# Kernel optimization log

Measured on AMD Instinct MI355X. Metric: run time of the kernel, lower is better.

Reference implementation:

```python
import jax, jax.numpy as jnp
import numpy as np

NUM_ITER = 3  # routing iterations (canonical CapsNet)
EPS = 1e-12


def _conv(x, w, stride):
    return jax.lax.conv_general_dilated(
        x, w, (stride, stride), 'VALID',
        dimension_numbers=('NCHW', 'OIHW', 'NCHW'))


def _squash(t, axis=-1):
    sn = (t * t).sum(axis=axis, keepdims=True)
    return sn / (1.0 + sn) * t / jnp.sqrt(sn + EPS)


def _batchnorm(x, eps=1e-5):
    # fresh BatchNorm2d in training mode: batch stats, weight=1, bias=0, biased var
    m = x.mean((0, 2, 3), keepdims=True)
    v = ((x - m) ** 2).mean((0, 2, 3), keepdims=True)
    return (x - m) * jax.lax.rsqrt(v + eps)


def _branch(x, cw, cb, pw, pb, rw):
    # x: [B,1,H,W]; cw: [128,1,k,k]; pw: [8,32,128,k,k]; rw: [10,R,8,16]
    y = jax.nn.relu(_conv(x, cw, 1) + cb[None, :, None, None])
    y = _batchnorm(y)
    nc, oc = pw.shape[0], pw.shape[1]  # 8 capsules, 32 channels each
    p = _conv(y, pw.reshape(nc * oc, pw.shape[2], pw.shape[3], pw.shape[4]), 2)
    p = p + pb.reshape(-1)[None, :, None, None]          # [B,256,h,w]
    B = p.shape[0]
    u = jnp.transpose(p.reshape(B, nc, -1), (0, 2, 1))   # [B,R,8], R=32*h*w
    u = _squash(u, axis=-1)
    priors = jnp.einsum('bri,nrio->nbro', u, rw)         # [10,B,R,16]
    b = jnp.zeros(priors.shape[:3] + (1,), priors.dtype)  # [10,B,R,1]
    for i in range(NUM_ITER):
        c = jax.nn.softmax(b, axis=2)                    # over route nodes
        v = _squash((c * priors).sum(axis=2, keepdims=True))  # [10,B,1,16]
        if i < NUM_ITER - 1:
            b = b + (priors * v).sum(axis=-1, keepdims=True)
    v = jnp.transpose(v[:, :, 0, :], (1, 0, 2))          # [B,10,16]
    return jnp.sqrt((v * v).sum(-1) + EPS)               # [B,10] capsule lengths


def setup_inputs() -> dict:
    key = jax.random.key(0)
    ks = jax.random.split(key, 16)
    s = 0.05
    return {
        'x': jax.random.normal(ks[0], (256, 1, 28, 28), jnp.float32),
        'conv1_w': jax.random.normal(ks[1], (128, 1, 3, 3), jnp.float32) * s,
        'conv1_b': jnp.zeros((128,), jnp.float32),
        'prim1_w': jax.random.normal(ks[2], (8, 32, 128, 3, 3), jnp.float32) * s,
        'prim1_b': jnp.zeros((8, 32), jnp.float32),
        'digit1_w': jax.random.normal(ks[3], (10, 128, 8, 16), jnp.float32),
        'conv2_w': jax.random.normal(ks[4], (128, 1, 5, 5), jnp.float32) * s,
        'conv2_b': jnp.zeros((128,), jnp.float32),
        'prim2_w': jax.random.normal(ks[5], (8, 32, 128, 5, 5), jnp.float32) * s,
        'prim2_b': jnp.zeros((8, 32), jnp.float32),
        'digit2_w': jax.random.normal(ks[6], (10, 288, 8, 16), jnp.float32),
        'conv3_w': jax.random.normal(ks[7], (128, 1, 9, 9), jnp.float32) * s,
        'conv3_b': jnp.zeros((128,), jnp.float32),
        'prim3_w': jax.random.normal(ks[8], (8, 32, 128, 9, 9), jnp.float32) * s,
        'prim3_b': jnp.zeros((8, 32), jnp.float32),
        'digit3_w': jax.random.normal(ks[9], (10, 1152, 8, 16), jnp.float32),
    }


def reference(x, conv1_w, conv1_b, prim1_w, prim1_b, digit1_w,
              conv2_w, conv2_b, prim2_w, prim2_b, digit2_w,
              conv3_w, conv3_b, prim3_w, prim3_b, digit3_w):
    img = x[:, 0]                                   # [B,28,28]
    B = img.shape[0]
    x3 = img                                        # 28x28
    x2 = img.reshape(B, 14, 2, 14, 2).mean((2, 4))  # 14x14 pyramid level
    x1 = x2.reshape(B, 7, 2, 7, 2).mean((2, 4))     # 7x7 pyramid level
    l1 = _branch(x1[:, None], conv1_w, conv1_b, prim1_w, prim1_b, digit1_w)
    l2 = _branch(x2[:, None], conv2_w, conv2_b, prim2_w, prim2_b, digit2_w)
    l3 = _branch(x3[:, None], conv3_w, conv3_b, prim3_w, prim3_b, digit3_w)
    return jax.nn.softmax(l1 + l2 + l3, axis=-1)    # [B,10]
```

## Files before the change

### kernel.cpp

```cpp
#include <hip/hip_runtime.h>
#include <math.h>

#define SQ_EPS 1e-12f
#define BN_EPS 1e-5f

typedef short short8 __attribute__((ext_vector_type(8)));
typedef float f32x4 __attribute__((ext_vector_type(4)));
typedef unsigned short ushort_t;

__device__ inline unsigned short f2bf(float x) {
    unsigned int u = __float_as_uint(x);
    unsigned int r = (u + 0x7fffu + ((u >> 16) & 1u)) >> 16;
    return (unsigned short)r;
}
__device__ inline float bf2f(unsigned short h) {
    return __uint_as_float(((unsigned int)h) << 16);
}

template<int IH, int IW, int KS, int OH, int OW>
__device__ void conv_body(const float* __restrict__ w, const float* __restrict__ bias,
                          ushort_t* __restrict__ yh, ushort_t* __restrict__ yl,
                          float* __restrict__ partial,
                          int b, int tid, float* s_img, float* s_w, float* s_red) {
    constexpr int KK = KS * KS;
    constexpr int OS = OH * OW;
    for (int i = tid; i < 128 * KK; i += 256) s_w[i] = w[i];
    __syncthreads();
    int c = tid & 127, half = tid >> 7;
    float bias_c = bias[c];
    float bsum = 0.f, bsq = 0.f;
    for (int r = half; r < OH; r += 2) {
        float acc[OW];
        #pragma unroll
        for (int j = 0; j < OW; ++j) acc[j] = bias_c;
        for (int u = 0; u < KS; ++u) {
            float rg[OW + KS - 1];
            #pragma unroll
            for (int j = 0; j < OW + KS - 1; ++j) rg[j] = s_img[(r + u) * IW + j];
            #pragma unroll
            for (int v = 0; v < KS; ++v) {
                float wv = s_w[c * KK + u * KS + v];
                #pragma unroll
                for (int j = 0; j < OW; ++j) acc[j] += wv * rg[j + v];
            }
        }
        #pragma unroll
        for (int j = 0; j < OW; ++j) {
            float val = fmaxf(acc[j], 0.f);
            bsum += val; bsq += val * val;
            unsigned short h = f2bf(val);
            unsigned short lo = f2bf(val - bf2f(h));
            int oidx = ((b * OS) + r * OW + j) * 128 + c;
            yh[oidx] = h; yl[oidx] = lo;
        }
    }
    s_red[tid] = bsum; __syncthreads();
    if (tid < 128) partial[b * 256 + c] = s_red[tid] + s_red[tid + 128];
    __syncthreads();
    s_red[tid] = bsq; __syncthreads();
    if (tid < 128) partial[b * 256 + 128 + c] = s_red[tid] + s_red[tid + 128];
}

__global__ __launch_bounds__(256) void conv_all_kernel(
        const float* __restrict__ img,
        const float* __restrict__ c1w, const float* __restrict__ c1b,
        const float* __restrict__ c2w, const float* __restrict__ c2b,
        const float* __restrict__ c3w, const float* __restrict__ c3b,
        ushort_t* __restrict__ yh1, ushort_t* __restrict__ yl1,
        ushort_t* __restrict__ yh2, ushort_t* __restrict__ yl2,
        ushort_t* __restrict__ yh3, ushort_t* __restrict__ yl3,
        float* __restrict__ partial_base) {
    __shared__ float s_img[784];
    __shared__ float s_tmp[196];
    __shared__ float s_w[128 * 81];
    __shared__ float s_red[256];
    int br = blockIdx.x >> 8, b = blockIdx.x & 255, tid = threadIdx.x;
    const float* im = img + b * 784;
    for (int i = tid; i < 784; i += 256) s_img[i] = im[i];
    __syncthreads();
    if (br <= 1) {
        for (int idx = tid; idx < 196; idx += 256) {
            int i = idx / 14, j = idx % 14;
            s_tmp[idx] = 0.25f * (s_img[(2*i)*28 + 2*j]   + s_img[(2*i)*28 + 2*j + 1] +
                                  s_img[(2*i+1)*28 + 2*j] + s_img[(2*i+1)*28 + 2*j + 1]);
        }
        __syncthreads();
        if (br == 0) {
            for (int idx = tid; idx < 49; idx += 256) {
                int i = idx / 7, j = idx % 7;
                s_img[idx] = 0.25f * (s_tmp[(2*i)*14 + 2*j]   + s_tmp[(2*i)*14 + 2*j + 1] +
                                      s_tmp[(2*i+1)*14 + 2*j] + s_tmp[(2*i+1)*14 + 2*j + 1]);
            }
        } else {
            for (int idx = tid; idx < 196; idx += 256) s_img[idx] = s_tmp[idx];
        }
        __syncthreads();
    }
    if (br == 0)      conv_body<7, 7, 3, 5, 5>(c1w, c1b, yh1, yl1, partial_base, b, tid, s_img, s_w, s_red);
    else if (br == 1) conv_body<14, 14, 5, 10, 10>(c2w, c2b, yh2, yl2, partial_base + 65536, b, tid, s_img, s_w, s_red);
    else              conv_body<28, 28, 9, 20, 20>(c3w, c3b, yh3, yl3, partial_base + 131072, b, tid, s_img, s_w, s_red);
}

__global__ void bn_final_kernel(const float* __restrict__ partial_base, float* __restrict__ bnp_base) {
    int br = blockIdx.x;
    const float* pp = partial_base + br * 65536;
    float* bnp = bnp_base + br * 512;
    float N = (br == 0) ? 6400.f : ((br == 1) ? 25600.f : 102400.f);
    int c = threadIdx.x;
    float s = 0.f, q = 0.f;
    for (int blk = 0; blk < 256; ++blk) {
        s += pp[blk * 256 + c];
        q += pp[blk * 256 + 128 + c];
    }
    float mean = s / N;
    float var = q / N - mean * mean;
    float inv = rsqrtf(var + BN_EPS);
    bnp[256 + c] = inv;
    bnp[384 + c] = -mean * inv;
}

__global__ __launch_bounds__(256) void wtrans_zero_kernel(
        const float* __restrict__ w1, const float* __restrict__ w2,
        const float* __restrict__ w3, const float* __restrict__ bnp_base,
        const float* __restrict__ pb1, const float* __restrict__ pb2,
        const float* __restrict__ pb3,
        ushort_t* __restrict__ wh1, ushort_t* __restrict__ wl1,
        ushort_t* __restrict__ wh2, ushort_t* __restrict__ wl2,
        ushort_t* __restrict__ wh3, ushort_t* __restrict__ wl3,
        float* __restrict__ b1, float* __restrict__ b2, float* __restrict__ b3,
        float* __restrict__ p3zero) {
    __shared__ float tile[128 * 81];
    __shared__ float r2[2];
    int blk = blockIdx.x, tid = threadIdx.x;
    if (blk >= 768) {
        ((float4*)p3zero)[(blk - 768) * 256 + tid] = (float4){0.f, 0.f, 0.f, 0.f};
        return;
    }
    int br = blk >> 8, ch = blk & 255;
    const float* w; const float* pb; ushort_t* wh; ushort_t* wl; float* bf; int KK;
    if (br == 0)      { w = w1; pb = pb1; wh = wh1; wl = wl1; bf = b1; KK = 9;  }
    else if (br == 1) { w = w2; pb = pb2; wh = wh2; wl = wl2; bf = b2; KK = 25; }
    else              { w = w3; pb = pb3; wh = wh3; wl = wl3; bf = b3; KK = 81; }
    const float* bnp = bnp_base + br * 512;
    int n = 128 * KK;
    const float* wrow = w + ch * n;
    for (int i = tid; i < n; i += 256) tile[i] = wrow[i];
    __syncthreads();
    for (int j = tid; j < n; j += 256) {
        int uv = j >> 7, c = j & 127;
        float val = tile[c * KK + uv] * bnp[256 + c];
        unsigned short h = f2bf(val);
        unsigned short lo = f2bf(val - bf2f(h));
        int oidx = uv * 32768 + (ch << 7) + c;
        wh[oidx] = h; wl[oidx] = lo;
    }
    float s = 0.f;
    if (tid < 128) {
        for (int uv = 0; uv < KK; ++uv) s += tile[tid * KK + uv];
        s *= bnp[384 + tid];
    }
    for (int off = 32; off; off >>= 1) s += __shfl_down(s, off);
    if (tid < 128 && (tid & 63) == 0) r2[tid >> 6] = s;
    __syncthreads();
    if (tid == 0) bf[ch] = pb[ch] + r2[0] + r2[1];
}

template<int S, int WO, int IHg, int IWg, int KS, int ZCH>
__device__ void gemm_body(const ushort_t* __restrict__ yh, const ushort_t* __restrict__ yl,
                          const ushort_t* __restrict__ wh, const ushort_t* __restrict__ wl,
                          float* __restrict__ p, int bx, int by, int bz, int tid,
                          ushort_t* Ash, ushort_t* Asl, ushort_t* Bsh, ushort_t* Bsl) {
    int bm = bx * 128, ch0 = by * 128;
    int arow = tid >> 2;
    int c0 = tid & 3;
    int sw0 = (c0 ^ ((arow >> 1) & 3)) * 8;
    int wA0 = arow * 32 + sw0;
    int wA1 = (arow + 64) * 32 + sw0;
    int m0 = bm + arow;
    int b0 = m0 / S, s0 = m0 % S;
    int abase0 = ((b0 * IHg + 2 * (s0 / WO)) * IWg + 2 * (s0 % WO)) * 128 + c0 * 8;
    int m1 = m0 + 64;
    int b1 = m1 / S, s1 = m1 % S;
    int abase1 = ((b1 * IHg + 2 * (s1 / WO)) * IWg + 2 * (s1 % WO)) * 128 + c0 * 8;
    int bbase0 = (ch0 + arow) * 128 + c0 * 8;
    int bbase1 = (ch0 + arow + 64) * 128 + c0 * 8;
    int lane = tid & 63, wid = tid >> 6;
    int wm = wid & 1, wn = wid >> 1;
    int quad = lane >> 4, l16 = lane & 15;
    int aoffL[4], boffL[4];
    #pragma unroll
    for (int mi = 0; mi < 4; ++mi) {
        int row = wm * 64 + mi * 16 + l16;
        aoffL[mi] = row * 32 + ((quad ^ ((row >> 1) & 3)) * 8);
    }
    #pragma unroll
    for (int ni = 0; ni < 4; ++ni) {
        int row = wn * 64 + ni * 16 + l16;
        boffL[ni] = row * 32 + ((quad ^ ((row >> 1) & 3)) * 8);
    }
    f32x4 acc[4][4];
    #pragma unroll
    for (int mi = 0; mi < 4; ++mi)
        #pragma unroll
        for (int ni = 0; ni < 4; ++ni)
            acc[mi][ni] = (f32x4){0.f, 0.f, 0.f, 0.f};

    int kc = bz * ZCH;
    int uv = kc >> 2, ci = kc & 3;
    int u = uv / KS, v = uv - u * KS;
    int aoff = (u * IWg + v) * 128 + (ci << 5);
    int boff = uv * 32768 + (ci << 5);
    int4 a0h = *reinterpret_cast<const int4*>(yh + abase0 + aoff);
    int4 a0l = *reinterpret_cast<const int4*>(yl + abase0 + aoff);
    int4 a1h = *reinterpret_cast<const int4*>(yh + abase1 + aoff);
    int4 a1l = *reinterpret_cast<const int4*>(yl + abase1 + aoff);
    int4 b0h = *reinterpret_cast<const int4*>(wh + bbase0 + boff);
    int4 b0l = *reinterpret_cast<const int4*>(wl + bbase0 + boff);
    int4 b1h = *reinterpret_cast<const int4*>(wh + bbase1 + boff);
    int4 b1l = *reinterpret_cast<const int4*>(wl + bbase1 + boff);

    for (int t = 0; t < ZCH; ++t) {
        __syncthreads();
        *reinterpret_cast<int4*>(&Ash[wA0]) = a0h;
        *reinterpret_cast<int4*>(&Asl[wA0]) = a0l;
        *reinterpret_cast<int4*>(&Ash[wA1]) = a1h;
        *reinterpret_cast<int4*>(&Asl[wA1]) = a1l;
        *reinterpret_cast<int4*>(&Bsh[wA0]) = b0h;
        *reinterpret_cast<int4*>(&Bsl[wA0]) = b0l;
        *reinterpret_cast<int4*>(&Bsh[wA1]) = b1h;
        *reinterpret_cast<int4*>(&Bsl[wA1]) = b1l;
        if (t + 1 < ZCH) {
            ci = (ci + 1) & 3;
            if (ci == 0) { ++uv; ++v; if (v == KS) { v = 0; ++u; } }
            aoff = (u * IWg + v) * 128 + (ci << 5);
            boff = uv * 32768 + (ci << 5);
            a0h = *reinterpret_cast<const int4*>(yh + abase0 + aoff);
            a0l = *reinterpret_cast<const int4*>(yl + abase0 + aoff);
            a1h = *reinterpret_cast<const int4*>(yh + abase1 + aoff);
            a1l = *reinterpret_cast<const int4*>(yl + abase1 + aoff);
            b0h = *reinterpret_cast<const int4*>(wh + bbase0 + boff);
            b0l = *reinterpret_cast<const int4*>(wl + bbase0 + boff);
            b1h = *reinterpret_cast<const int4*>(wh + bbase1 + boff);
            b1l = *reinterpret_cast<const int4*>(wl + bbase1 + boff);
        }
        __syncthreads();
        short8 bh[4], bl[4];
        #pragma unroll
        for (int ni = 0; ni < 4; ++ni) {
            bh[ni] = *reinterpret_cast<const short8*>(&Bsh[boffL[ni]]);
            bl[ni] = *reinterpret_cast<const short8*>(&Bsl[boffL[ni]]);
        }
        #pragma unroll
        for (int mi = 0; mi < 4; ++mi) {
            short8 ah = *reinterpret_cast<const short8*>(&Ash[aoffL[mi]]);
            short8 al = *reinterpret_cast<const short8*>(&Asl[aoffL[mi]]);
            #pragma unroll
            for (int ni = 0; ni < 4; ++ni) {
                acc[mi][ni] = __builtin_amdgcn_mfma_f32_16x16x32_bf16(ah, bh[ni], acc[mi][ni], 0, 0, 0);
                acc[mi][ni] = __builtin_amdgcn_mfma_f32_16x16x32_bf16(al, bh[ni], acc[mi][ni], 0, 0, 0);
                acc[mi][ni] = __builtin_amdgcn_mfma_f32_16x16x32_bf16(ah, bl[ni], acc[mi][ni], 0, 0, 0);
            }
        }
    }
    #pragma unroll
    for (int mi = 0; mi < 4; ++mi)
        #pragma unroll
        for (int ni = 0; ni < 4; ++ni) {
            int col = ch0 + wn * 64 + ni * 16 + l16;
            #pragma unroll
            for (int reg = 0; reg < 4; ++reg) {
                int row = bm + wm * 64 + mi * 16 + quad * 4 + reg;
                atomicAdd(p + (size_t)row * 256 + col, acc[mi][ni][reg]);
            }
        }
}

__global__ __launch_bounds__(256, 3) void gemm3_kernel(
        const ushort_t* __restrict__ yh, const ushort_t* __restrict__ yl,
        const ushort_t* __restrict__ wh, const ushort_t* __restrict__ wl,
        float* __restrict__ p) {
    __shared__ ushort_t Ash[128 * 32], Asl[128 * 32];
    __shared__ ushort_t Bsh[128 * 32], Bsl[128 * 32];
    gemm_body<36, 6, 20, 20, 9, 54>(yh, yl, wh, wl, p,
                                    blockIdx.x, blockIdx.y, blockIdx.z, threadIdx.x,
                                    Ash, Asl, Bsh, Bsl);
}

__global__ __launch_bounds__(256, 3) void gemm21_kernel(
        const ushort_t* __restrict__ yh2, const ushort_t* __restrict__ yl2,
        const ushort_t* __restrict__ wh2, const ushort_t* __restrict__ wl2, float* __restrict__ p2,
        const ushort_t* __restrict__ yh1, const ushort_t* __restrict__ yl1,
        const ushort_t* __restrict__ wh1, const ushort_t* __restrict__ wl1, float* __restrict__ p1) {
    __shared__ ushort_t Ash[128 * 32], Asl[128 * 32];
    __shared__ ushort_t Bsh[128 * 32], Bsl[128 * 32];
    int blk = blockIdx.x, tid = threadIdx.x;
    if (blk < 360) {
        int z = blk / 36, rem = blk % 36, y = rem / 18, x = rem % 18;
        gemm_body<9, 3, 10, 10, 5, 10>(yh2, yl2, wh2, wl2, p2, x, y, z, tid, Ash, Asl, Bsh, Bsl);
    } else {
        int b = blk - 360;
        int z = b / 16, rem = b % 16, y = rem / 8, x = rem % 8;
        gemm_body<4, 2, 5, 5, 3, 4>(yh1, yl1, wh1, wl1, p1, x, y, z, tid, Ash, Asl, Bsh, Bsl);
    }
}

__global__ void squash_all_kernel(const float* __restrict__ p1, const float* __restrict__ p2,
                                  const float* __restrict__ p3,
                                  const float* __restrict__ bias1, const float* __restrict__ bias2,
                                  const float* __restrict__ bias3,
                                  float* __restrict__ u1, float* __restrict__ u2,
                                  float* __restrict__ u3) {
    int blk = blockIdx.x;
    const float* p; const float* bias; float* u; int S;
    if (blk < 128)      { p = p1; bias = bias1; u = u1; S = 4; }
    else if (blk < 416) { p = p2; bias = bias2; u = u2; S = 9;  blk -= 128; }
    else                { p = p3; bias = bias3; u = u3; S = 36; blk -= 416; }
    int idx = blk * 256 + threadIdx.x;
    int o = idx & 31, rest = idx >> 5;
    int s = rest % S, b = rest / S;
    const float* pp = p + (size_t)(b * S + s) * 256 + o;
    float t[8]; float sn = 0.f;
    #pragma unroll
    for (int i = 0; i < 8; ++i) { t[i] = pp[i * 32] + bias[o + i * 32]; sn += t[i] * t[i]; }
    float f = sn / ((1.f + sn) * sqrtf(sn + SQ_EPS));
    float* up = u + (size_t)(b * (32 * S) + o * S + s) * 8;
    float4 w0 = {t[0] * f, t[1] * f, t[2] * f, t[3] * f};
    float4 w1 = {t[4] * f, t[5] * f, t[6] * f, t[7] * f};
    *reinterpret_cast<float4*>(up) = w0;
    *reinterpret_cast<float4*>(up + 4) = w1;
}

__global__ void rwtrans_zero_kernel(const float* __restrict__ w1, const float* __restrict__ w2,
                                    const float* __restrict__ w3,
                                    float* __restrict__ o1, float* __restrict__ o2,
                                    float* __restrict__ o3,
                                    float* __restrict__ p2, float* __restrict__ p1) {
    int blk = blockIdx.x;
    if (blk >= 7840) {
        int zb = blk - 7840;
        if (zb < 576) ((float4*)p2)[zb * 256 + threadIdx.x] = (float4){0.f, 0.f, 0.f, 0.f};
        else          ((float4*)p1)[(zb - 576) * 256 + threadIdx.x] = (float4){0.f, 0.f, 0.f, 0.f};
        return;
    }
    int idx = blk * 256 + threadIdx.x;
    if (idx < 163840) {
        int t = idx;
        int jj = t & 3; t >>= 2;
        int r = t & 127; t >>= 7;
        int g2 = t & 31; int n = t >> 5;
        o1[idx] = w1[(n * 128 + r) * 128 + g2 * 4 + jj];
    } else if (idx < 532480) {
        int t = idx - 163840;
        int jj = t & 3; t >>= 2;
        int r = t % 288; t /= 288;
        int g2 = t & 31; int n = t >> 5;
        o2[idx - 163840] = w2[(n * 288 + r) * 128 + g2 * 4 + jj];
    } else {
        int t = idx - 532480;
        int jj = t & 3; t >>= 2;
        int r = t % 1152; t /= 1152;
        int g2 = t & 31; int n = t >> 5;
        o3[idx - 532480] = w3[(n * 1152 + r) * 128 + g2 * 4 + jj];
    }
}

template<int R>
__device__ void routing_body(const float* __restrict__ u, const float* __restrict__ rwt,
                             float* __restrict__ lens, int n, int b, int tid,
                             float* red, float* vsh, float* sred) {
    constexpr int KMAX = (R + 255) / 256;
    constexpr float invR = 1.0f / (float)R;
    int lane = tid & 63, wv = tid >> 6;

    unsigned int d[KMAX][8];
    float a[16];
    float blog[KMAX];
    float v[16];

    #pragma unroll
    for (int o = 0; o < 16; ++o) a[o] = 0.f;
    #pragma unroll
    for (int k = 0; k < KMAX; ++k) blog[k] = 0.f;

    #pragma unroll
    for (int k = 0; k < KMAX; ++k) {
        int r = tid + k * 256;
        if (r < R) {
            const float4* up = (const float4*)(u + ((size_t)b * R + r) * 8);
            float4 ua = up[0], ub2 = up[1];
            float uu[8] = {ua.x, ua.y, ua.z, ua.w, ub2.x, ub2.y, ub2.z, ub2.w};
            float po[16];
            #pragma unroll
            for (int o = 0; o < 16; ++o) po[o] = 0.f;
            #pragma unroll
            for (int g2 = 0; g2 < 32; ++g2) {
                float4 w4 = *reinterpret_cast<const float4*>(rwt + (((size_t)n * 32 + g2) * R + r) * 4);
                float ui = uu[g2 >> 2];
                int o0 = (g2 & 3) * 4;
                po[o0 + 0] += ui * w4.x;
                po[o0 + 1] += ui * w4.y;
                po[o0 + 2] += ui * w4.z;
                po[o0 + 3] += ui * w4.w;
            }
            #pragma unroll
            for (int j = 0; j < 8; ++j)
                d[k][j] = (unsigned int)f2bf(po[2*j]) | ((unsigned int)f2bf(po[2*j+1]) << 16);
            #pragma unroll
            for (int o = 0; o < 16; ++o) a[o] += po[o];
        }
    }

    for (int it = 0; it < 3; ++it) {
        if (it > 0) {
            float lsum = 0.f;
            #pragma unroll
            for (int o = 0; o < 16; ++o) a[o] = 0.f;
            #pragma unroll
            for (int k = 0; k < KMAX; ++k) {
                int r = tid + k * 256;
                if (r < R) {
                    float pv[16];
                    #pragma unroll
                    for (int j = 0; j < 8; ++j) {
                        pv[2*j]   = __uint_as_float(d[k][j] << 16);
                        pv[2*j+1] = __uint_as_float(d[k][j] & 0xffff0000u);
                    }
                    float dt0 = 0.f, dt1 = 0.f, dt2 = 0.f, dt3 = 0.f;
                    #pragma unroll
                    for (int o = 0; o < 4; ++o) {
                        dt0 += pv[o]      * v[o];
                        dt1 += pv[4 + o]  * v[4 + o];
                        dt2 += pv[8 + o]  * v[8 + o];
                        dt3 += pv[12 + o] * v[12 + o];
                    }
                    blog[k] += (dt0 + dt1) + (dt2 + dt3);
                    float e = __expf(blog[k]);
                    lsum += e;
                    #pragma unroll
                    for (int o = 0; o < 16; ++o) a[o] += e * pv[o];
                }
            }
            lsum += __shfl_xor(lsum, 1);
            lsum += __shfl_xor(lsum, 2);
            lsum += __shfl_xor(lsum, 4);
            lsum += __shfl_xor(lsum, 8);
            lsum += __shfl_xor(lsum, 16);
            lsum += __shfl_xor(lsum, 32);
            if (lane == 0) sred[wv] = lsum;
        }
        #pragma unroll
        for (int k2 = 0; k2 < 4; ++k2) {
            int m = 1 << k2;
            int lb = (lane >> k2) & 1;
            #pragma unroll
            for (int t = 0; t < (8 >> k2); ++t) {
                float x0 = a[2 * t], x1 = a[2 * t + 1];
                float keep = lb ? x1 : x0;
                float send = lb ? x0 : x1;
                a[t] = keep + __shfl_xor(send, m);
            }
        }
        float tot = a[0];
        tot += __shfl_xor(tot, 16);
        tot += __shfl_xor(tot, 32);
        if (lane < 16) red[wv * 16 + lane] = tot;
        __syncthreads();
        if (tid < 16) {
            float vo = red[tid] + red[16 + tid] + red[32 + tid] + red[48 + tid];
            float scale = (it == 0) ? invR
                                    : 1.0f / (sred[0] + sred[1] + sred[2] + sred[3]);
            vo *= scale;
            float sn = vo * vo;
            sn += __shfl_xor(sn, 1);
            sn += __shfl_xor(sn, 2);
            sn += __shfl_xor(sn, 4);
            sn += __shfl_xor(sn, 8);
            float f = sn / ((1.f + sn) * sqrtf(sn + SQ_EPS));
            if (it == 2) {
                if (tid == 0) lens[b * 10 + n] = sqrtf(sn * f * f + SQ_EPS);
            } else {
                vsh[tid] = vo * f;
            }
        }
        __syncthreads();
        if (it < 2) {
            #pragma unroll
            for (int o = 0; o < 16; ++o) v[o] = vsh[o];
        }
    }
}

__global__ __launch_bounds__(256, 4) void routing_all_kernel(
        const float* __restrict__ u1, const float* __restrict__ u2, const float* __restrict__ u3,
        const float* __restrict__ rwt1, const float* __restrict__ rwt2,
        const float* __restrict__ rwt3,
        float* __restrict__ l1, float* __restrict__ l2, float* __restrict__ l3) {
    __shared__ float red[64];
    __shared__ float vsh[16];
    __shared__ float sred[4];
    int n = blockIdx.x, b = blockIdx.y, br = 2 - blockIdx.z, tid = threadIdx.x;
    if (br == 0)      routing_body<128>(u1, rwt1, l1, n, b, tid, red, vsh, sred);
    else if (br == 1) routing_body<288>(u2, rwt2, l2, n, b, tid, red, vsh, sred);
    else              routing_body<1152>(u3, rwt3, l3, n, b, tid, red, vsh, sred);
}

__global__ void final_softmax_kernel(const float* __restrict__ l1, const float* __restrict__ l2,
                                     const float* __restrict__ l3, float* __restrict__ out) {
    int b = threadIdx.x;
    float v[10]; float mx = -1e30f;
    #pragma unroll
    for (int n = 0; n < 10; ++n) {
        v[n] = l1[b * 10 + n] + l2[b * 10 + n] + l3[b * 10 + n];
        mx = fmaxf(mx, v[n]);
    }
    float s = 0.f;
    #pragma unroll
    for (int n = 0; n < 10; ++n) { v[n] = expf(v[n] - mx); s += v[n]; }
    float inv = 1.f / s;
    #pragma unroll
    for (int n = 0; n < 10; ++n) out[b * 10 + n] = v[n] * inv;
}

extern "C" void kernel_launch(void* const* d_in, const int* in_sizes, int n_in,
                              void* d_out, int out_size, void* d_ws, size_t ws_size,
                              hipStream_t stream) {
    const float* x   = (const float*)d_in[0];
    const float* c1w = (const float*)d_in[1];
    const float* c1b = (const float*)d_in[2];
    const float* p1w = (const float*)d_in[3];
    const float* p1b = (const float*)d_in[4];
    const float* d1w = (const float*)d_in[5];
    const float* c2w = (const float*)d_in[6];
    const float* c2b = (const float*)d_in[7];
    const float* p2w = (const float*)d_in[8];
    const float* p2b = (const float*)d_in[9];
    const float* d2w = (const float*)d_in[10];
    const float* c3w = (const float*)d_in[11];
    const float* c3b = (const float*)d_in[12];
    const float* p3w = (const float*)d_in[13];
    const float* p3b = (const float*)d_in[14];
    const float* d3w = (const float*)d_in[15];

    float* ws = (float*)d_ws;
    float* yh1f  = ws + 62720;
    float* yl1f  = ws + 472320;
    float* yh2f  = ws + 881920;
    float* yl2f  = ws + 2520320;
    float* yh3f  = ws + 4158720;
    float* yl3f  = ws + 10712320;
    float* wh1f  = ws + 17265920;
    float* wl1f  = ws + 17413376;
    float* wh2f  = ws + 17560832;
    float* wl2f  = ws + 17970432;
    float* wh3f  = ws + 18380032;
    float* wl3f  = ws + 19707136;
    float* p3    = ws + 21034240;
    float* bnp1  = ws + 23393536;
    float* bias1 = ws + 23395072;
    float* bias2 = ws + 23395328;
    float* bias3 = ws + 23395584;
    float* l1    = ws + 23395840;
    float* l2    = ws + 23398400;
    float* l3    = ws + 23400960;

    ushort_t* yh1 = (ushort_t*)yh1f; ushort_t* yl1 = (ushort_t*)yl1f;
    ushort_t* yh2 = (ushort_t*)yh2f; ushort_t* yl2 = (ushort_t*)yl2f;
    ushort_t* yh3 = (ushort_t*)yh3f; ushort_t* yl3 = (ushort_t*)yl3f;
    ushort_t* wh1 = (ushort_t*)wh1f; ushort_t* wl1 = (ushort_t*)wl1f;
    ushort_t* wh2 = (ushort_t*)wh2f; ushort_t* wl2 = (ushort_t*)wl2f;
    ushort_t* wh3 = (ushort_t*)wh3f; ushort_t* wl3 = (ushort_t*)wl3f;
    float* u1 = yh1f;
    float* u2 = yh2f;
    float* u3 = yh3f;
    float* p2 = wh3f;
    float* p1 = wl3f;
    float* rwt1 = yl3f;
    float* rwt2 = rwt1 + 163840;
    float* rwt3 = rwt2 + 368640;

    conv_all_kernel<<<768, 256, 0, stream>>>(x, c1w, c1b, c2w, c2b, c3w, c3b,
                                             yh1, yl1, yh2, yl2, yh3, yl3, p3);
    bn_final_kernel<<<3, 128, 0, stream>>>(p3, bnp1);
    wtrans_zero_kernel<<<3072, 256, 0, stream>>>(p1w, p2w, p3w, bnp1, p1b, p2b, p3b,
                                                 wh1, wl1, wh2, wl2, wh3, wl3,
                                                 bias1, bias2, bias3, p3);
    gemm3_kernel<<<dim3(72, 2, 6), 256, 0, stream>>>(yh3, yl3, wh3, wl3, p3);
    rwtrans_zero_kernel<<<8672, 256, 0, stream>>>(d1w, d2w, d3w, rwt1, rwt2, rwt3, p2, p1);
    gemm21_kernel<<<504, 256, 0, stream>>>(yh2, yl2, wh2, wl2, p2, yh1, yl1, wh1, wl1, p1);
    squash_all_kernel<<<1568, 256, 0, stream>>>(p1, p2, p3, bias1, bias2, bias3, u1, u2, u3);
    routing_all_kernel<<<dim3(10, 256, 3), 256, 0, stream>>>(u1, u2, u3, rwt1, rwt2, rwt3, l1, l2, l3);
    final_softmax_kernel<<<1, 256, 0, stream>>>(l1, l2, l3, (float*)d_out);
}
```

Measured before the change: 549.9 us.

## Double-buffer GEMM tiles with direct global-to-LDS loads and XCD block swizzle

Measured after the change: 536.6 us. 1.02x faster.

```diff
diff --git a/kernel.cpp b/kernel.cpp
--- a/kernel.cpp
+++ b/kernel.cpp
@@ -15,6 +15,13 @@
 }
 __device__ inline float bf2f(unsigned short h) {
     return __uint_as_float(((unsigned int)h) << 16);
+}
+
+__device__ inline void gload_lds16(const ushort_t* g, ushort_t* l) {
+    __builtin_amdgcn_global_load_lds(
+        (const __attribute__((address_space(1))) void*)(g),
+        (__attribute__((address_space(3))) void*)(l),
+        16, 0, 0);
 }
 
 template<int IH, int IW, int KS, int OH, int OW>
@@ -173,19 +180,19 @@
     int bm = bx * 128, ch0 = by * 128;
     int arow = tid >> 2;
     int c0 = tid & 3;
-    int sw0 = (c0 ^ ((arow >> 1) & 3)) * 8;
-    int wA0 = arow * 32 + sw0;
-    int wA1 = (arow + 64) * 32 + sw0;
+    int c0s = c0 ^ ((arow >> 1) & 3);
+    int lane = tid & 63, wid = tid >> 6;
+    int wb0 = wid * 512;
+    int wb1 = 64 * 32 + wid * 512;
     int m0 = bm + arow;
     int b0 = m0 / S, s0 = m0 % S;
-    int abase0 = ((b0 * IHg + 2 * (s0 / WO)) * IWg + 2 * (s0 % WO)) * 128 + c0 * 8;
+    int abase0 = ((b0 * IHg + 2 * (s0 / WO)) * IWg + 2 * (s0 % WO)) * 128 + c0s * 8;
     int m1 = m0 + 64;
     int b1 = m1 / S, s1 = m1 % S;
-    int abase1 = ((b1 * IHg + 2 * (s1 / WO)) * IWg + 2 * (s1 % WO)) * 128 + c0 * 8;
-    int bbase0 = (ch0 + arow) * 128 + c0 * 8;
-    int bbase1 = (ch0 + arow + 64) * 128 + c0 * 8;
-    int lane = tid & 63, wid = tid >> 6;
-    int wm = wid & 1, wn = wid >> 1;
+    int abase1 = ((b1 * IHg + 2 * (s1 / WO)) * IWg + 2 * (s1 % WO)) * 128 + c0s * 8;
+    int bbase0 = (ch0 + arow) * 128 + c0s * 8;
+    int bbase1 = (ch0 + arow + 64) * 128 + c0s * 8;
+    int wm = (tid >> 6) & 1, wn = tid >> 7;
     int quad = lane >> 4, l16 = lane & 15;
     int aoffL[4], boffL[4];
     #pragma unroll
@@ -210,50 +217,39 @@
     int u = uv / KS, v = uv - u * KS;
     int aoff = (u * IWg + v) * 128 + (ci << 5);
     int boff = uv * 32768 + (ci << 5);
-    int4 a0h = *reinterpret_cast<const int4*>(yh + abase0 + aoff);
-    int4 a0l = *reinterpret_cast<const int4*>(yl + abase0 + aoff);
-    int4 a1h = *reinterpret_cast<const int4*>(yh + abase1 + aoff);
-    int4 a1l = *reinterpret_cast<const int4*>(yl + abase1 + aoff);
-    int4 b0h = *reinterpret_cast<const int4*>(wh + bbase0 + boff);
-    int4 b0l = *reinterpret_cast<const int4*>(wl + bbase0 + boff);
-    int4 b1h = *reinterpret_cast<const int4*>(wh + bbase1 + boff);
-    int4 b1l = *reinterpret_cast<const int4*>(wl + bbase1 + boff);
+
+    #define GEMM_ADV() do { ci = (ci + 1) & 3;                                   \
+        if (ci == 0) { ++uv; ++v; if (v == KS) { v = 0; ++u; } }                 \
+        aoff = (u * IWg + v) * 128 + (ci << 5);                                  \
+        boff = uv * 32768 + (ci << 5); } while (0)
+    #define GEMM_ISSUE(BSEL) do { int o_ = (BSEL) * 4096;                        \
+        gload_lds16(yh + abase0 + aoff, Ash + o_ + wb0);                         \
+        gload_lds16(yl + abase0 + aoff, Asl + o_ + wb0);                         \
+        gload_lds16(yh + abase1 + aoff, Ash + o_ + wb1);                         \
+        gload_lds16(yl + abase1 + aoff, Asl + o_ + wb1);                         \
+        gload_lds16(wh + bbase0 + boff, Bsh + o_ + wb0);                         \
+        gload_lds16(wl + bbase0 + boff, Bsl + o_ + wb0);                         \
+        gload_lds16(wh + bbase1 + boff, Bsh + o_ + wb1);                         \
+        gload_lds16(wl + bbase1 + boff, Bsl + o_ + wb1); } while (0)
+
+    GEMM_ISSUE(0); GEMM_ADV();
+    GEMM_ISSUE(1); GEMM_ADV();
 
     for (int t = 0; t < ZCH; ++t) {
-        __syncthreads();
-        *reinterpret_cast<int4*>(&Ash[wA0]) = a0h;
-        *reinterpret_cast<int4*>(&Asl[wA0]) = a0l;
-        *reinterpret_cast<int4*>(&Ash[wA1]) = a1h;
-        *reinterpret_cast<int4*>(&Asl[wA1]) = a1l;
-        *reinterpret_cast<int4*>(&Bsh[wA0]) = b0h;
-        *reinterpret_cast<int4*>(&Bsl[wA0]) = b0l;
-        *reinterpret_cast<int4*>(&Bsh[wA1]) = b1h;
-        *reinterpret_cast<int4*>(&Bsl[wA1]) = b1l;
-        if (t + 1 < ZCH) {
-            ci = (ci + 1) & 3;
-            if (ci == 0) { ++uv; ++v; if (v == KS) { v = 0; ++u; } }
-            aoff = (u * IWg + v) * 128 + (ci << 5);
-            boff = uv * 32768 + (ci << 5);
-            a0h = *reinterpret_cast<const int4*>(yh + abase0 + aoff);
-            a0l = *reinterpret_cast<const int4*>(yl + abase0 + aoff);
-            a1h = *reinterpret_cast<const int4*>(yh + abase1 + aoff);
-            a1l = *reinterpret_cast<const int4*>(yl + abase1 + aoff);
-            b0h = *reinterpret_cast<const int4*>(wh + bbase0 + boff);
-            b0l = *reinterpret_cast<const int4*>(wl + bbase0 + boff);
-            b1h = *reinterpret_cast<const int4*>(wh + bbase1 + boff);
-            b1l = *reinterpret_cast<const int4*>(wl + bbase1 + boff);
-        }
-        __syncthreads();
+        if (t < ZCH - 1) { asm volatile("s_waitcnt vmcnt(8)" ::: "memory"); }
+        else             { asm volatile("s_waitcnt vmcnt(0)" ::: "memory"); }
+        asm volatile("s_barrier" ::: "memory");
+        int bo = (t & 1) * 4096;
         short8 bh[4], bl[4];
         #pragma unroll
         for (int ni = 0; ni < 4; ++ni) {
-            bh[ni] = *reinterpret_cast<const short8*>(&Bsh[boffL[ni]]);
-            bl[ni] = *reinterpret_cast<const short8*>(&Bsl[boffL[ni]]);
+            bh[ni] = *reinterpret_cast<const short8*>(&Bsh[bo + boffL[ni]]);
+            bl[ni] = *reinterpret_cast<const short8*>(&Bsl[bo + boffL[ni]]);
         }
         #pragma unroll
         for (int mi = 0; mi < 4; ++mi) {
-            short8 ah = *reinterpret_cast<const short8*>(&Ash[aoffL[mi]]);
-            short8 al = *reinterpret_cast<const short8*>(&Asl[aoffL[mi]]);
+            short8 ah = *reinterpret_cast<const short8*>(&Ash[bo + aoffL[mi]]);
+            short8 al = *reinterpret_cast<const short8*>(&Asl[bo + aoffL[mi]]);
             #pragma unroll
             for (int ni = 0; ni < 4; ++ni) {
                 acc[mi][ni] = __builtin_amdgcn_mfma_f32_16x16x32_bf16(ah, bh[ni], acc[mi][ni], 0, 0, 0);
@@ -261,7 +257,15 @@
                 acc[mi][ni] = __builtin_amdgcn_mfma_f32_16x16x32_bf16(ah, bl[ni], acc[mi][ni], 0, 0, 0);
             }
         }
-    }
+        asm volatile("s_barrier" ::: "memory");
+        if (t + 3 <= ZCH) {
+            GEMM_ISSUE(t & 1);
+            GEMM_ADV();
+        }
+    }
+    #undef GEMM_ISSUE
+    #undef GEMM_ADV
+
     #pragma unroll
     for (int mi = 0; mi < 4; ++mi)
         #pragma unroll
@@ -275,30 +279,35 @@
         }
 }
 
-__global__ __launch_bounds__(256, 3) void gemm3_kernel(
+__global__ __launch_bounds__(256, 2) void gemm3_kernel(
         const ushort_t* __restrict__ yh, const ushort_t* __restrict__ yl,
         const ushort_t* __restrict__ wh, const ushort_t* __restrict__ wl,
         float* __restrict__ p) {
-    __shared__ ushort_t Ash[128 * 32], Asl[128 * 32];
-    __shared__ ushort_t Bsh[128 * 32], Bsl[128 * 32];
+    __shared__ ushort_t Ash[2 * 4096], Asl[2 * 4096];
+    __shared__ ushort_t Bsh[2 * 4096], Bsl[2 * 4096];
+    int bid = blockIdx.x + 72 * (blockIdx.y + 2 * blockIdx.z);
+    int swz = (bid & 7) * 108 + (bid >> 3);
+    int x = swz % 72, r = swz / 72;
     gemm_body<36, 6, 20, 20, 9, 54>(yh, yl, wh, wl, p,
-                                    blockIdx.x, blockIdx.y, blockIdx.z, threadIdx.x,
+                                    x, r & 1, r >> 1, threadIdx.x,
                                     Ash, Asl, Bsh, Bsl);
 }
 
-__global__ __launch_bounds__(256, 3) void gemm21_kernel(
+__global__ __launch_bounds__(256, 2) void gemm21_kernel(
         const ushort_t* __restrict__ yh2, const ushort_t* __restrict__ yl2,
         const ushort_t* __restrict__ wh2, const ushort_t* __restrict__ wl2, float* __restrict__ p2,
         const ushort_t* __restrict__ yh1, const ushort_t* __restrict__ yl1,
         const ushort_t* __restrict__ wh1, const ushort_t* __restrict__ wl1, float* __restrict__ p1) {
-    __shared__ ushort_t Ash[128 * 32], Asl[128 * 32];
-    __shared__ ushort_t Bsh[128 * 32], Bsl[128 * 32];
-    int blk = blockIdx.x, tid = threadIdx.x;
-    if (blk < 360) {
-        int z = blk / 36, rem = blk % 36, y = rem / 18, x = rem % 18;
+    __shared__ ushort_t Ash[2 * 4096], Asl[2 * 4096];
+    __shared__ ushort_t Bsh[2 * 4096], Bsl[2 * 4096];
+    int bid = blockIdx.x;
+    int swz = (bid & 7) * 63 + (bid >> 3);
+    int tid = threadIdx.x;
+    if (swz < 360) {
+        int z = swz / 36, rem = swz % 36, y = rem / 18, x = rem % 18;
         gemm_body<9, 3, 10, 10, 5, 10>(yh2, yl2, wh2, wl2, p2, x, y, z, tid, Ash, Asl, Bsh, Bsl);
     } else {
-        int b = blk - 360;
+        int b = swz - 360;
         int z = b / 16, rem = b % 16, y = rem / 8, x = rem % 8;
         gemm_body<4, 2, 5, 5, 3, 4>(yh1, yl1, wh1, wl1, p1, x, y, z, tid, Ash, Asl, Bsh, Bsl);
     }
```
